# Optimization experiments

Hardware: AMD Instinct MI355X
Metric: run time of the kernel (lower is better)

## Reference

```python
import jax, jax.numpy as jnp
import numpy as np

BN_EPS = 1e-5

def setup_inputs() -> dict:
    key = jax.random.key(0)
    ks = jax.random.split(key, 8)
    C = 64
    NB, N_SP = 256, 64          # num blocks, spatial n (size3d = (1, 64, 64))
    N = NB * N_SP * N_SP        # 1,048,576 total rows
    s = np.sqrt(2.0 / C).astype(np.float32)   # kaiming_normal fan_in scale
    s2 = np.sqrt(2.0 / (2 * C)).astype(np.float32)
    return {
        "x":   jax.random.normal(ks[0], (N, C), jnp.float32),
        "w11": jax.random.normal(ks[1], (C, C), jnp.float32) * s,
        "b11": jnp.zeros((C,), jnp.float32),
        "w12": jax.random.normal(ks[2], (C, C), jnp.float32) * s,
        "b12": jnp.zeros((C,), jnp.float32),
        "w21": jax.random.normal(ks[3], (C, C), jnp.float32) * s,
        "b21": jnp.zeros((C,), jnp.float32),
        "w22": jax.random.normal(ks[4], (C, C), jnp.float32) * s,
        "b22": jnp.zeros((C,), jnp.float32),
        "uW1": jax.random.normal(ks[5], (2 * C, C), jnp.float32) * s2,
        "ub1": jnp.zeros((C,), jnp.float32),
        "g1":  jnp.ones((C,), jnp.float32),
        "be1": jnp.zeros((C,), jnp.float32),
        "uW2": jax.random.normal(ks[6], (C, C), jnp.float32) * s,
        "ub2": jnp.zeros((C,), jnp.float32),
        "g2":  jnp.ones((C,), jnp.float32),
        "be2": jnp.zeros((C,), jnp.float32),
        "num_blocks": NB,
        "blk_n": N_SP,
    }

def _block_mlp(h, params):
    # 1x1 Conv2d stack == per-position channel matmul; W is (out_ch, in_ch)
    for W, b in params:
        h = jax.nn.relu(jnp.einsum('bijc,oc->bijo', h, W) + b)
    return h

def _bn_relu(z, g, b):
    # BatchNorm1d, training mode: batch mean / biased batch var
    mu = jnp.mean(z, axis=0)
    var = jnp.var(z, axis=0)
    return jax.nn.relu((z - mu) * jax.lax.rsqrt(var + BN_EPS) * g + b)

def reference(x, w11, b11, w12, b12, w21, b21, w22, b22,
              uW1, ub1, g1, be1, uW2, ub2, g2, be2, num_blocks, blk_n):
    C = x.shape[-1]
    # uniform blocks: split + reshape to (b=1, n, n, C) -> fold into one array
    xb = x.reshape(num_blocks, blk_n, blk_n, C)          # NHWC (block, i, j, c)
    m1 = _block_mlp(xb, [(w11, b11), (w12, b12)])
    m2 = _block_mlp(xb, [(w21, b21), (w22, b22)])
    # torch.matmul over trailing spatial dims, batched over (block, channel)
    corr = jnp.einsum('bikc,bkjc->bijc', m1, m2)
    h = jnp.sqrt(jax.nn.relu(corr)).reshape(-1, C)
    h = jnp.concatenate([x, h], axis=1)                  # [N, 2C]
    h = _bn_relu(h @ uW1 + ub1, g1, be1)
    h = _bn_relu(h @ uW2 + ub2, g2, be2)
    return h + x
```

## Files before the change

kernel.cpp:

```cpp
#include <hip/hip_runtime.h>

#define NROWS   1048576
#define SBLK    4096

using bfrag = __attribute__((ext_vector_type(8))) short;
using ffrag = __attribute__((ext_vector_type(4))) float;
using uifrag = __attribute__((ext_vector_type(4))) unsigned;

__device__ __forceinline__ float bf2f(unsigned short u) {
    unsigned w = ((unsigned)u) << 16;
    return __builtin_bit_cast(float, w);
}
__device__ __forceinline__ unsigned short f2bf(float f) {
    unsigned u = __builtin_bit_cast(unsigned, f);
    u += 0x7fffu + ((u >> 16) & 1u);
    return (unsigned short)(u >> 16);
}
__device__ __forceinline__ short pk(float f) { return (short)f2bf(f); }
__device__ __forceinline__ unsigned cvtpk(float lo, float hi) {
    unsigned r;
    asm("v_cvt_pk_bf16_f32 %0, %1, %2" : "=v"(r) : "v"(lo), "v"(hi));
    return r;
}

__global__ void k_prep(const float* __restrict__ w11, const float* __restrict__ w12,
                       const float* __restrict__ w21, const float* __restrict__ w22,
                       const float* __restrict__ uW1, const float* __restrict__ uW2,
                       unsigned short* __restrict__ w11b, unsigned short* __restrict__ w12b,
                       unsigned short* __restrict__ w21b, unsigned short* __restrict__ w22b,
                       unsigned short* __restrict__ uW1bt, unsigned short* __restrict__ uW2bt)
{
    int t = threadIdx.x;
    for (int i = t; i < 4096; i += 256) {
        w11b[i] = f2bf(w11[i]);
        w12b[i] = f2bf(w12[i]);
        w21b[i] = f2bf(w21[i]);
        w22b[i] = f2bf(w22[i]);
        int o = i >> 6, c = i & 63;
        uW2bt[o * 64 + c] = f2bf(uW2[c * 64 + o]);
    }
    for (int i = t; i < 8192; i += 256) {
        int o = i >> 7, c = i & 127;
        uW1bt[o * 128 + c] = f2bf(uW1[c * 64 + o]);
    }
}

__global__ __launch_bounds__(256, 3) void k_mlp(
    const float* __restrict__ x,
    const unsigned short* __restrict__ w11b, const float* __restrict__ b11,
    const unsigned short* __restrict__ w12b, const float* __restrict__ b12,
    const unsigned short* __restrict__ w21b, const float* __restrict__ b21,
    const unsigned short* __restrict__ w22b, const float* __restrict__ b22,
    unsigned short* __restrict__ M1, unsigned short* __restrict__ M2)
{
    __shared__ unsigned short ts[4][64 * 72];
    const int t   = threadIdx.x;
    const int w   = t >> 6, ln = t & 63;
    const int col = ln & 15, q = ln >> 4;
    unsigned short* tsw = ts[w];

    const int nw = gridDim.x * 4;
    for (int tile = blockIdx.x * 4 + w; tile < NROWS / 64; tile += nw) {
        const int n0 = tile * 64;
        const int b = n0 >> 12, s0 = n0 & (SBLK - 1);

        bfrag ax[4][2];
        #pragma unroll
        for (int mt = 0; mt < 4; ++mt) {
            const float* xr = x + (size_t)(n0 + mt * 16 + col) * 64 + q * 8;
            #pragma unroll
            for (int kt = 0; kt < 2; ++kt) {
                float4 lo = *reinterpret_cast<const float4*>(xr + kt * 32);
                float4 hi = *reinterpret_cast<const float4*>(xr + kt * 32 + 4);
                uifrag u;
                u[0] = cvtpk(lo.x, lo.y);
                u[1] = cvtpk(lo.z, lo.w);
                u[2] = cvtpk(hi.x, hi.y);
                u[3] = cvtpk(hi.z, hi.w);
                ax[mt][kt] = __builtin_bit_cast(bfrag, u);
            }
        }

        #pragma unroll
        for (int br = 0; br < 2; ++br) {
            const unsigned short* wA = br ? w21b : w11b;
            const unsigned short* wB = br ? w22b : w12b;
            const float* bA = br ? b21 : b11;
            const float* bB = br ? b22 : b12;
            unsigned short* Mb = (br ? M2 : M1) + ((size_t)b << 18) + s0;

            bfrag  bw[4][2];
            float4 bsv[4];
            #pragma unroll
            for (int ot = 0; ot < 4; ++ot) {
                #pragma unroll
                for (int kt = 0; kt < 2; ++kt)
                    bw[ot][kt] = *reinterpret_cast<const bfrag*>(
                        wA + (ot * 16 + col) * 64 + kt * 32 + q * 8);
                bsv[ot] = *reinterpret_cast<const float4*>(bA + ot * 16 + q * 4);
            }
            #pragma unroll
            for (int mt = 0; mt < 4; ++mt) {
                #pragma unroll
                for (int ot = 0; ot < 4; ++ot) {
                    ffrag acc = {0.f, 0.f, 0.f, 0.f};
                    acc = __builtin_amdgcn_mfma_f32_16x16x32_bf16(bw[ot][0], ax[mt][0], acc, 0, 0, 0);
                    acc = __builtin_amdgcn_mfma_f32_16x16x32_bf16(bw[ot][1], ax[mt][1], acc, 0, 0, 0);
                    float4 bs = bsv[ot];
                    unsigned u0 = cvtpk(fmaxf(acc[0] + bs.x, 0.f), fmaxf(acc[1] + bs.y, 0.f));
                    unsigned u1 = cvtpk(fmaxf(acc[2] + bs.z, 0.f), fmaxf(acc[3] + bs.w, 0.f));
                    *reinterpret_cast<uint2*>(&tsw[(mt * 16 + col) * 72 + ot * 16 + q * 4]) =
                        make_uint2(u0, u1);
                }
            }
            #pragma unroll
            for (int ot = 0; ot < 4; ++ot) {
                #pragma unroll
                for (int kt = 0; kt < 2; ++kt)
                    bw[ot][kt] = *reinterpret_cast<const bfrag*>(
                        wB + (ot * 16 + col) * 64 + kt * 32 + q * 8);
                bsv[ot] = *reinterpret_cast<const float4*>(bB + ot * 16 + q * 4);
            }
            #pragma unroll
            for (int mt = 0; mt < 4; ++mt) {
                bfrag az0 = *reinterpret_cast<const bfrag*>(&tsw[(mt * 16 + col) * 72 + q * 8]);
                bfrag az1 = *reinterpret_cast<const bfrag*>(&tsw[(mt * 16 + col) * 72 + 32 + q * 8]);
                #pragma unroll
                for (int ot = 0; ot < 4; ++ot) {
                    ffrag acc = {0.f, 0.f, 0.f, 0.f};
                    acc = __builtin_amdgcn_mfma_f32_16x16x32_bf16(bw[ot][0], az0, acc, 0, 0, 0);
                    acc = __builtin_amdgcn_mfma_f32_16x16x32_bf16(bw[ot][1], az1, acc, 0, 0, 0);
                    float4 bs = bsv[ot];
                    unsigned u0 = cvtpk(fmaxf(acc[0] + bs.x, 0.f), fmaxf(acc[1] + bs.y, 0.f));
                    unsigned u1 = cvtpk(fmaxf(acc[2] + bs.z, 0.f), fmaxf(acc[3] + bs.w, 0.f));
                    unsigned short* mp = Mb + (size_t)(ot * 16 + q * 4) * SBLK + mt * 16 + col;
                    mp[0]        = (unsigned short)u0;
                    mp[SBLK]     = (unsigned short)(u0 >> 16);
                    mp[2 * SBLK] = (unsigned short)u1;
                    mp[3 * SBLK] = (unsigned short)(u1 >> 16);
                }
            }
        }
    }
}

__global__ __launch_bounds__(256, 4) void k_corr(
    unsigned short* __restrict__ M1, const unsigned short* __restrict__ M2)
{
    __shared__ unsigned short Bt[4][64 * 72];
    const int t   = threadIdx.x;
    const int w   = t >> 6, ln = t & 63;
    const int col = ln & 15, q = ln >> 4;
    const size_t cb = (size_t)blockIdx.x << 14;

    const int k = t >> 2, j0 = (t & 3) * 16;
    #pragma unroll
    for (int cc = 0; cc < 4; ++cc) {
        const unsigned short* Bc = M2 + cb + cc * 4096 + (size_t)k * 64 + j0;
        uint4 p0 = reinterpret_cast<const uint4*>(Bc)[0];
        uint4 p1 = reinterpret_cast<const uint4*>(Bc)[1];
        unsigned pv[8] = { p0.x, p0.y, p0.z, p0.w, p1.x, p1.y, p1.z, p1.w };
        #pragma unroll
        for (int m = 0; m < 8; ++m) {
            Bt[cc][(j0 + 2 * m) * 72 + k]     = (unsigned short)(pv[m] & 0xffff);
            Bt[cc][(j0 + 2 * m + 1) * 72 + k] = (unsigned short)(pv[m] >> 16);
        }
    }
    __syncthreads();

    #pragma unroll
    for (int cc = 0; cc < 4; ++cc) {
        unsigned short* Ac = M1 + cb + cc * 4096;
        bfrag a0 = *reinterpret_cast<const bfrag*>(Ac + (w * 16 + col) * 64 + q * 8);
        bfrag a1 = *reinterpret_cast<const bfrag*>(Ac + (w * 16 + col) * 64 + 32 + q * 8);
        #pragma unroll
        for (int nj = 0; nj < 4; ++nj) {
            bfrag bq0 = *reinterpret_cast<const bfrag*>(&Bt[cc][(nj * 16 + col) * 72 + q * 8]);
            bfrag bq1 = *reinterpret_cast<const bfrag*>(&Bt[cc][(nj * 16 + col) * 72 + 32 + q * 8]);
            ffrag acc = {0.f, 0.f, 0.f, 0.f};
            acc = __builtin_amdgcn_mfma_f32_16x16x32_bf16(a0, bq0, acc, 0, 0, 0);
            acc = __builtin_amdgcn_mfma_f32_16x16x32_bf16(a1, bq1, acc, 0, 0, 0);
            unsigned u0 = cvtpk(sqrtf(fmaxf(acc[0], 0.f)), sqrtf(fmaxf(acc[1], 0.f)));
            unsigned u1 = cvtpk(sqrtf(fmaxf(acc[2], 0.f)), sqrtf(fmaxf(acc[3], 0.f)));
            unsigned short* hp = Ac + (size_t)(w * 16 + q * 4) * 64 + nj * 16 + col;
            hp[0]   = (unsigned short)u0;
            hp[64]  = (unsigned short)(u0 >> 16);
            hp[128] = (unsigned short)u1;
            hp[192] = (unsigned short)(u1 >> 16);
        }
    }
}

__global__ __launch_bounds__(256) void k_fc1(
    const float* __restrict__ x, const unsigned short* __restrict__ H,
    const unsigned short* __restrict__ uW1bt, const float* __restrict__ ub1,
    unsigned short* __restrict__ Z1, float* __restrict__ sum1, float* __restrict__ sq1)
{
    __shared__ unsigned short hs[4][16 * 72];
    __shared__ float redS[4][64], redQ[4][64];
    const int t   = threadIdx.x;
    const int w   = t >> 6, ln = t & 63;
    const int col = ln & 15, q = ln >> 4;
    unsigned short* hsw = hs[w];

    bfrag bw[4][4];
    #pragma unroll
    for (int kt = 0; kt < 4; ++kt)
        #pragma unroll
        for (int ct = 0; ct < 4; ++ct)
            bw[kt][ct] = *reinterpret_cast<const bfrag*>(
                uW1bt + (ct * 16 + col) * 128 + kt * 32 + q * 8);
    float bias[4];
    #pragma unroll
    for (int ct = 0; ct < 4; ++ct) bias[ct] = ub1[ct * 16 + col];

    float sA[4] = {0, 0, 0, 0}, qA[4] = {0, 0, 0, 0};

    for (int blk = blockIdx.x; blk < NROWS / 64; blk += gridDim.x) {
        const int n0 = blk * 64;
        const int b = n0 >> 12, s0 = n0 & (SBLK - 1);

        {
            const unsigned short* hp = H + ((size_t)b << 18) + (size_t)ln * SBLK + s0 + w * 16;
            uint4 p0 = reinterpret_cast<const uint4*>(hp)[0];
            uint4 p1 = reinterpret_cast<const uint4*>(hp)[1];
            unsigned pv[8] = { p0.x, p0.y, p0.z, p0.w, p1.x, p1.y, p1.z, p1.w };
            #pragma unroll
            for (int m = 0; m < 8; ++m) {
                hsw[(2 * m + 0) * 72 + ln] = (unsigned short)(pv[m] & 0xffff);
                hsw[(2 * m + 1) * 72 + ln] = (unsigned short)(pv[m] >> 16);
            }
        }

        const int row = w * 16 + col;
        bfrag ax[2];
        #pragma unroll
        for (int kt = 0; kt < 2; ++kt) {
            const float* xp = x + (size_t)(n0 + row) * 64 + kt * 32 + q * 8;
            float4 lo = reinterpret_cast<const float4*>(xp)[0];
            float4 hi = reinterpret_cast<const float4*>(xp)[1];
            uifrag u;
            u[0] = cvtpk(lo.x, lo.y);
            u[1] = cvtpk(lo.z, lo.w);
            u[2] = cvtpk(hi.x, hi.y);
            u[3] = cvtpk(hi.z, hi.w);
            ax[kt] = __builtin_bit_cast(bfrag, u);
        }
        bfrag ah0 = *reinterpret_cast<const bfrag*>(&hsw[col * 72 + q * 8]);
        bfrag ah1 = *reinterpret_cast<const bfrag*>(&hsw[col * 72 + 32 + q * 8]);

        #pragma unroll
        for (int ct = 0; ct < 4; ++ct) {
            ffrag acc = {0.f, 0.f, 0.f, 0.f};
            acc = __builtin_amdgcn_mfma_f32_16x16x32_bf16(ax[0], bw[0][ct], acc, 0, 0, 0);
            acc = __builtin_amdgcn_mfma_f32_16x16x32_bf16(ax[1], bw[1][ct], acc, 0, 0, 0);
            acc = __builtin_amdgcn_mfma_f32_16x16x32_bf16(ah0,  bw[2][ct], acc, 0, 0, 0);
            acc = __builtin_amdgcn_mfma_f32_16x16x32_bf16(ah1,  bw[3][ct], acc, 0, 0, 0);
            #pragma unroll
            for (int r = 0; r < 4; ++r) {
                float v = acc[r] + bias[ct];
                Z1[(size_t)(n0 + w * 16 + q * 4 + r) * 64 + ct * 16 + col] = f2bf(v);
                sA[ct] += v; qA[ct] += v * v;
            }
        }
    }

    #pragma unroll
    for (int ct = 0; ct < 4; ++ct) {
        float s = sA[ct], qq = qA[ct];
        s  += __shfl_xor(s, 16);  s  += __shfl_xor(s, 32);
        qq += __shfl_xor(qq, 16); qq += __shfl_xor(qq, 32);
        if (q == 0) { redS[w][ct * 16 + col] = s; redQ[w][ct * 16 + col] = qq; }
    }
    __syncthreads();
    if (t < 64) {
        float S = redS[0][t] + redS[1][t] + redS[2][t] + redS[3][t];
        float Q = redQ[0][t] + redQ[1][t] + redQ[2][t] + redQ[3][t];
        atomicAdd(&sum1[t], S);
        atomicAdd(&sq1[t], Q);
    }
}

__global__ void k_final(const float* __restrict__ sum, const float* __restrict__ sq,
                        const float* __restrict__ g, const float* __restrict__ be,
                        float* __restrict__ scale, float* __restrict__ shift)
{
    int c = threadIdx.x;
    if (c < 64) {
        const float invN = 1.f / (float)NROWS;
        float mu  = sum[c] * invN;
        float var = sq[c] * invN - mu * mu;
        float rs  = rsqrtf(var + 1e-5f);
        float sc  = g[c] * rs;
        scale[c] = sc;
        shift[c] = be[c] - mu * sc;
    }
}

__global__ __launch_bounds__(256) void k_fc2(
    const unsigned short* __restrict__ Z1, const unsigned short* __restrict__ uW2bt,
    const float* __restrict__ ub2, const float* __restrict__ scale1,
    const float* __restrict__ shift1,
    unsigned short* __restrict__ Z2, float* __restrict__ sum2, float* __restrict__ sq2)
{
    __shared__ float redS[4][64], redQ[4][64];
    const int t   = threadIdx.x;
    const int w   = t >> 6, ln = t & 63;
    const int col = ln & 15, q = ln >> 4;

    bfrag bw[2][4];
    #pragma unroll
    for (int kt = 0; kt < 2; ++kt)
        #pragma unroll
        for (int ct = 0; ct < 4; ++ct)
            bw[kt][ct] = *reinterpret_cast<const bfrag*>(
                uW2bt + (ct * 16 + col) * 64 + kt * 32 + q * 8);
    float bias[4];
    #pragma unroll
    for (int ct = 0; ct < 4; ++ct) bias[ct] = ub2[ct * 16 + col];
    float sc[2][8], sh[2][8];
    #pragma unroll
    for (int kt = 0; kt < 2; ++kt)
        #pragma unroll
        for (int j = 0; j < 8; ++j) {
            int c = kt * 32 + q * 8 + j;
            sc[kt][j] = scale1[c];
            sh[kt][j] = shift1[c];
        }

    float sA[4] = {0, 0, 0, 0}, qA[4] = {0, 0, 0, 0};

    const int wg = blockIdx.x * 4 + w;
    const int stride = gridDim.x * 4;
    for (int tile = wg; tile < NROWS / 16; tile += stride) {
        const size_t rbase = (size_t)tile * 16;
        bfrag a[2];
        #pragma unroll
        for (int kt = 0; kt < 2; ++kt) {
            const unsigned short* zp = Z1 + (rbase + col) * 64 + kt * 32 + q * 8;
            uint4 p = *reinterpret_cast<const uint4*>(zp);
            unsigned pv[4] = { p.x, p.y, p.z, p.w };
            bfrag av;
            #pragma unroll
            for (int m = 0; m < 4; ++m) {
                float lo = bf2f((unsigned short)(pv[m] & 0xffff));
                float hi = bf2f((unsigned short)(pv[m] >> 16));
                lo = fmaxf(fmaf(lo, sc[kt][2 * m],     sh[kt][2 * m]),     0.f);
                hi = fmaxf(fmaf(hi, sc[kt][2 * m + 1], sh[kt][2 * m + 1]), 0.f);
                av[2 * m] = pk(lo); av[2 * m + 1] = pk(hi);
            }
            a[kt] = av;
        }
        #pragma unroll
        for (int ct = 0; ct < 4; ++ct) {
            ffrag acc = {0.f, 0.f, 0.f, 0.f};
            acc = __builtin_amdgcn_mfma_f32_16x16x32_bf16(a[0], bw[0][ct], acc, 0, 0, 0);
            acc = __builtin_amdgcn_mfma_f32_16x16x32_bf16(a[1], bw[1][ct], acc, 0, 0, 0);
            #pragma unroll
            for (int r = 0; r < 4; ++r) {
                float v = acc[r] + bias[ct];
                Z2[(rbase + q * 4 + r) * 64 + ct * 16 + col] = f2bf(v);
                sA[ct] += v; qA[ct] += v * v;
            }
        }
    }

    #pragma unroll
    for (int ct = 0; ct < 4; ++ct) {
        float s = sA[ct], qq = qA[ct];
        s  += __shfl_xor(s, 16);  s  += __shfl_xor(s, 32);
        qq += __shfl_xor(qq, 16); qq += __shfl_xor(qq, 32);
        if (q == 0) { redS[w][ct * 16 + col] = s; redQ[w][ct * 16 + col] = qq; }
    }
    __syncthreads();
    if (t < 64) {
        float S = redS[0][t] + redS[1][t] + redS[2][t] + redS[3][t];
        float Q = redQ[0][t] + redQ[1][t] + redQ[2][t] + redQ[3][t];
        atomicAdd(&sum2[t], S);
        atomicAdd(&sq2[t], Q);
    }
}

__global__ __launch_bounds__(256) void k_out(
    const float* __restrict__ x, const unsigned short* __restrict__ Z2,
    const float* __restrict__ scale2, const float* __restrict__ shift2,
    float* __restrict__ out)
{
    const int i  = blockIdx.x * 256 + threadIdx.x;
    const int c0 = (i & 15) * 4;
    float4 xv = reinterpret_cast<const float4*>(x)[i];
    ushort4 zv = reinterpret_cast<const ushort4*>(Z2)[i];
    float4 o;
    o.x = fmaxf(fmaf(bf2f(zv.x), scale2[c0 + 0], shift2[c0 + 0]), 0.f) + xv.x;
    o.y = fmaxf(fmaf(bf2f(zv.y), scale2[c0 + 1], shift2[c0 + 1]), 0.f) + xv.y;
    o.z = fmaxf(fmaf(bf2f(zv.z), scale2[c0 + 2], shift2[c0 + 2]), 0.f) + xv.z;
    o.w = fmaxf(fmaf(bf2f(zv.w), scale2[c0 + 3], shift2[c0 + 3]), 0.f) + xv.w;
    reinterpret_cast<float4*>(out)[i] = o;
}

extern "C" void kernel_launch(void* const* d_in, const int* in_sizes, int n_in,
                              void* d_out, int out_size, void* d_ws, size_t ws_size,
                              hipStream_t stream)
{
    const float* x   = (const float*)d_in[0];
    const float* w11 = (const float*)d_in[1];
    const float* b11 = (const float*)d_in[2];
    const float* w12 = (const float*)d_in[3];
    const float* b12 = (const float*)d_in[4];
    const float* w21 = (const float*)d_in[5];
    const float* b21 = (const float*)d_in[6];
    const float* w22 = (const float*)d_in[7];
    const float* b22 = (const float*)d_in[8];
    const float* uW1 = (const float*)d_in[9];
    const float* ub1 = (const float*)d_in[10];
    const float* g1  = (const float*)d_in[11];
    const float* be1 = (const float*)d_in[12];
    const float* uW2 = (const float*)d_in[13];
    const float* ub2 = (const float*)d_in[14];
    const float* g2  = (const float*)d_in[15];
    const float* be2 = (const float*)d_in[16];

    char* ws = (char*)d_ws;
    const size_t BUF = (size_t)NROWS * 64 * sizeof(unsigned short);
    unsigned short* B0 = (unsigned short*)ws;
    unsigned short* B1 = (unsigned short*)(ws + BUF);
    float* stats  = (float*)(ws + 2 * BUF);
    float* sum1   = stats;        float* sq1    = stats + 64;
    float* sum2   = stats + 128;  float* sq2    = stats + 192;
    float* scale1 = stats + 256;  float* shift1 = stats + 320;
    float* scale2 = stats + 384;  float* shift2 = stats + 448;
    unsigned short* wb = (unsigned short*)(ws + 2 * BUF + 2048);
    unsigned short* w11b  = wb;
    unsigned short* w12b  = wb + 4096;
    unsigned short* w21b  = wb + 8192;
    unsigned short* w22b  = wb + 12288;
    unsigned short* uW1bt = wb + 16384;
    unsigned short* uW2bt = wb + 24576;

    hipMemsetAsync(stats, 0, 256 * sizeof(float), stream);

    k_prep<<<1, 256, 0, stream>>>(w11, w12, w21, w22, uW1, uW2,
                                  w11b, w12b, w21b, w22b, uW1bt, uW2bt);
    k_mlp<<<2048, 256, 0, stream>>>(x, w11b, b11, w12b, b12, w21b, b21, w22b, b22, B0, B1);
    k_corr<<<4096, 256, 0, stream>>>(B0, B1);
    k_fc1<<<2048, 256, 0, stream>>>(x, B0, uW1bt, ub1, B1, sum1, sq1);
    k_final<<<1, 64, 0, stream>>>(sum1, sq1, g1, be1, scale1, shift1);
    k_fc2<<<2048, 256, 0, stream>>>(B1, uW2bt, ub2, scale1, shift1, B0, sum2, sq2);
    k_final<<<1, 64, 0, stream>>>(sum2, sq2, g2, be2, scale2, shift2);
    k_out<<<NROWS * 64 / 4 / 256, 256, 0, stream>>>(x, B0, scale2, shift2, (float*)d_out);
}
```

Baseline: 998.4 us.

## Stream MLP rows per subtile, fold bias into MFMA accumulator, per-wave corr

k_mlp now loads and converts x one 16-row subtile at a time instead of holding all four, keeps both layer weight fragments resident, and initializes the accumulator with the bias instead of adding it afterwards. This cuts per-wave LDS scratch from 64 to 16 rows and raises the occupancy hint from 3 to 4 blocks. k_corr now gives each wave one channel matrix, so it transposes its own B into its own LDS slice with packed 32-bit writes and no block barrier. The risk is that holding both weight sets raises register pressure, and the per-subtile loop may expose more global-load latency.

```diff
diff --git a/kernel.cpp b/kernel.cpp
--- a/kernel.cpp
+++ b/kernel.cpp
@@ -45,7 +45,7 @@
     }
 }
 
-__global__ __launch_bounds__(256, 3) void k_mlp(
+__global__ __launch_bounds__(256, 4) void k_mlp(
     const float* __restrict__ x,
     const unsigned short* __restrict__ w11b, const float* __restrict__ b11,
     const unsigned short* __restrict__ w12b, const float* __restrict__ b12,
@@ -53,7 +53,7 @@
     const unsigned short* __restrict__ w22b, const float* __restrict__ b22,
     unsigned short* __restrict__ M1, unsigned short* __restrict__ M2)
 {
-    __shared__ unsigned short ts[4][64 * 72];
+    __shared__ unsigned short ts[4][16 * 72];
     const int t   = threadIdx.x;
     const int w   = t >> 6, ln = t & 63;
     const int col = ln & 15, q = ln >> 4;
@@ -63,23 +63,6 @@
     for (int tile = blockIdx.x * 4 + w; tile < NROWS / 64; tile += nw) {
         const int n0 = tile * 64;
         const int b = n0 >> 12, s0 = n0 & (SBLK - 1);
-
-        bfrag ax[4][2];
-        #pragma unroll
-        for (int mt = 0; mt < 4; ++mt) {
-            const float* xr = x + (size_t)(n0 + mt * 16 + col) * 64 + q * 8;
-            #pragma unroll
-            for (int kt = 0; kt < 2; ++kt) {
-                float4 lo = *reinterpret_cast<const float4*>(xr + kt * 32);
-                float4 hi = *reinterpret_cast<const float4*>(xr + kt * 32 + 4);
-                uifrag u;
-                u[0] = cvtpk(lo.x, lo.y);
-                u[1] = cvtpk(lo.z, lo.w);
-                u[2] = cvtpk(hi.x, hi.y);
-                u[3] = cvtpk(hi.z, hi.w);
-                ax[mt][kt] = __builtin_bit_cast(bfrag, u);
-            }
-        }
 
         #pragma unroll
         for (int br = 0; br < 2; ++br) {
@@ -89,50 +72,63 @@
             const float* bB = br ? b22 : b12;
             unsigned short* Mb = (br ? M2 : M1) + ((size_t)b << 18) + s0;
 
-            bfrag  bw[4][2];
-            float4 bsv[4];
+            bfrag w1f[4][2], w2f[4][2];
             #pragma unroll
-            for (int ot = 0; ot < 4; ++ot) {
+            for (int ot = 0; ot < 4; ++ot)
                 #pragma unroll
-                for (int kt = 0; kt < 2; ++kt)
-                    bw[ot][kt] = *reinterpret_cast<const bfrag*>(
+                for (int kt = 0; kt < 2; ++kt) {
+                    w1f[ot][kt] = *reinterpret_cast<const bfrag*>(
                         wA + (ot * 16 + col) * 64 + kt * 32 + q * 8);
-                bsv[ot] = *reinterpret_cast<const float4*>(bA + ot * 16 + q * 4);
-            }
-            #pragma unroll
+                    w2f[ot][kt] = *reinterpret_cast<const bfrag*>(
+                        wB + (ot * 16 + col) * 64 + kt * 32 + q * 8);
+                }
+
             for (int mt = 0; mt < 4; ++mt) {
+                const float* xr = x + (size_t)(n0 + mt * 16 + col) * 64 + q * 8;
+                bfrag ax0, ax1;
+                {
+                    float4 lo = *reinterpret_cast<const float4*>(xr);
+                    float4 hi = *reinterpret_cast<const float4*>(xr + 4);
+                    uifrag u;
+                    u[0] = cvtpk(lo.x, lo.y);
+                    u[1] = cvtpk(lo.z, lo.w);
+                    u[2] = cvtpk(hi.x, hi.y);
+                    u[3] = cvtpk(hi.z, hi.w);
+                    ax0 = __builtin_bit_cast(bfrag, u);
+                }
+                {
+                    float4 lo = *reinterpret_cast<const float4*>(xr + 32);
+                    float4 hi = *reinterpret_cast<const float4*>(xr + 36);
+                    uifrag u;
+                    u[0] = cvtpk(lo.x, lo.y);
+                    u[1] = cvtpk(lo.z, lo.w);
+                    u[2] = cvtpk(hi.x, hi.y);
+                    u[3] = cvtpk(hi.z, hi.w);
+                    ax1 = __builtin_bit_cast(bfrag, u);
+                }
+
                 #pragma unroll
                 for (int ot = 0; ot < 4; ++ot) {
-                    ffrag acc = {0.f, 0.f, 0.f, 0.f};
-                    acc = __builtin_amdgcn_mfma_f32_16x16x32_bf16(bw[ot][0], ax[mt][0], acc, 0, 0, 0);
-                    acc = __builtin_amdgcn_mfma_f32_16x16x32_bf16(bw[ot][1], ax[mt][1], acc, 0, 0, 0);
-                    float4 bs = bsv[ot];
-                    unsigned u0 = cvtpk(fmaxf(acc[0] + bs.x, 0.f), fmaxf(acc[1] + bs.y, 0.f));
-                    unsigned u1 = cvtpk(fmaxf(acc[2] + bs.z, 0.f), fmaxf(acc[3] + bs.w, 0.f));
-                    *reinterpret_cast<uint2*>(&tsw[(mt * 16 + col) * 72 + ot * 16 + q * 4]) =
+                    float4 bv = *reinterpret_cast<const float4*>(bA + ot * 16 + q * 4);
+                    ffrag acc = {bv.x, bv.y, bv.z, bv.w};
+                    acc = __builtin_amdgcn_mfma_f32_16x16x32_bf16(w1f[ot][0], ax0, acc, 0, 0, 0);
+                    acc = __builtin_amdgcn_mfma_f32_16x16x32_bf16(w1f[ot][1], ax1, acc, 0, 0, 0);
+                    unsigned u0 = cvtpk(fmaxf(acc[0], 0.f), fmaxf(acc[1], 0.f));
+                    unsigned u1 = cvtpk(fmaxf(acc[2], 0.f), fmaxf(acc[3], 0.f));
+                    *reinterpret_cast<uint2*>(&tsw[col * 72 + ot * 16 + q * 4]) =
                         make_uint2(u0, u1);
                 }
-            }
-            #pragma unroll
-            for (int ot = 0; ot < 4; ++ot) {
-                #pragma unroll
-                for (int kt = 0; kt < 2; ++kt)
-                    bw[ot][kt] = *reinterpret_cast<const bfrag*>(
-                        wB + (ot * 16 + col) * 64 + kt * 32 + q * 8);
-                bsv[ot] = *reinterpret_cast<const float4*>(bB + ot * 16 + q * 4);
-            }
-            #pragma unroll
-            for (int mt = 0; mt < 4; ++mt) {
-                bfrag az0 = *reinterpret_cast<const bfrag*>(&tsw[(mt * 16 + col) * 72 + q * 8]);
-                bfrag az1 = *reinterpret_cast<const bfrag*>(&tsw[(mt * 16 + col) * 72 + 32 + q * 8]);
+                bfrag az0 = *reinterpret_cast<const bfrag*>(&tsw[col * 72 + q * 8]);
+                bfrag az1 = *reinterpret_cast<const bfrag*>(&tsw[col * 72 + 32 + q * 8]);
+
                 #pragma unroll
                 for (int ot = 0; ot < 4; ++ot) {
-                    ffrag acc = {0.f, 0.f, 0.f, 0.f};
-                    acc = __builtin_amdgcn_mfma_f32_16x16x32_bf16(bw[ot][0], az0, acc, 0, 0, 0);
-                    acc = __builtin_amdgcn_mfma_f32_16x16x32_bf16(bw[ot][1], az1, acc, 0, 0, 0);
-                    float4 bs = bsv[ot];
-                    unsigned u0 = cvtpk(fmaxf(acc[0] + bs.x, 0.f), fmaxf(acc[1] + bs.y, 0.f));
-                    unsigned u1 = cvtpk(fmaxf(acc[2] + bs.z, 0.f), fmaxf(acc[3] + bs.w, 0.f));
+                    float4 bv = *reinterpret_cast<const float4*>(bB + ot * 16 + q * 4);
+                    ffrag acc = {bv.x, bv.y, bv.z, bv.w};
+                    acc = __builtin_amdgcn_mfma_f32_16x16x32_bf16(w2f[ot][0], az0, acc, 0, 0, 0);
+                    acc = __builtin_amdgcn_mfma_f32_16x16x32_bf16(w2f[ot][1], az1, acc, 0, 0, 0);
+                    unsigned u0 = cvtpk(fmaxf(acc[0], 0.f), fmaxf(acc[1], 0.f));
+                    unsigned u1 = cvtpk(fmaxf(acc[2], 0.f), fmaxf(acc[3], 0.f));
                     unsigned short* mp = Mb + (size_t)(ot * 16 + q * 4) * SBLK + mt * 16 + col;
                     mp[0]        = (unsigned short)u0;
                     mp[SBLK]     = (unsigned short)(u0 >> 16);
@@ -151,38 +147,48 @@
     const int t   = threadIdx.x;
     const int w   = t >> 6, ln = t & 63;
     const int col = ln & 15, q = ln >> 4;
-    const size_t cb = (size_t)blockIdx.x << 14;
-
-    const int k = t >> 2, j0 = (t & 3) * 16;
-    #pragma unroll
-    for (int cc = 0; cc < 4; ++cc) {
-        const unsigned short* Bc = M2 + cb + cc * 4096 + (size_t)k * 64 + j0;
-        uint4 p0 = reinterpret_cast<const uint4*>(Bc)[0];
-        uint4 p1 = reinterpret_cast<const uint4*>(Bc)[1];
-        unsigned pv[8] = { p0.x, p0.y, p0.z, p0.w, p1.x, p1.y, p1.z, p1.w };
-        #pragma unroll
-        for (int m = 0; m < 8; ++m) {
-            Bt[cc][(j0 + 2 * m) * 72 + k]     = (unsigned short)(pv[m] & 0xffff);
-            Bt[cc][(j0 + 2 * m + 1) * 72 + k] = (unsigned short)(pv[m] >> 16);
-        }
-    }
-    __syncthreads();
-
-    #pragma unroll
-    for (int cc = 0; cc < 4; ++cc) {
-        unsigned short* Ac = M1 + cb + cc * 4096;
-        bfrag a0 = *reinterpret_cast<const bfrag*>(Ac + (w * 16 + col) * 64 + q * 8);
-        bfrag a1 = *reinterpret_cast<const bfrag*>(Ac + (w * 16 + col) * 64 + 32 + q * 8);
+    unsigned short* Bw = Bt[w];
+    const size_t cb = ((size_t)(blockIdx.x * 4 + w)) << 12;
+
+    {
+        const int a = ln & 31, half = ln >> 5;
+        const unsigned short* Bc = M2 + cb + (size_t)(2 * a) * 64 + half * 32;
+        uint4 r0a = reinterpret_cast<const uint4*>(Bc)[0];
+        uint4 r0b = reinterpret_cast<const uint4*>(Bc)[1];
+        uint4 r0c = reinterpret_cast<const uint4*>(Bc)[2];
+        uint4 r0d = reinterpret_cast<const uint4*>(Bc)[3];
+        uint4 r1a = reinterpret_cast<const uint4*>(Bc + 64)[0];
+        uint4 r1b = reinterpret_cast<const uint4*>(Bc + 64)[1];
+        uint4 r1c = reinterpret_cast<const uint4*>(Bc + 64)[2];
+        uint4 r1d = reinterpret_cast<const uint4*>(Bc + 64)[3];
+        unsigned p0[16] = { r0a.x, r0a.y, r0a.z, r0a.w, r0b.x, r0b.y, r0b.z, r0b.w,
+                            r0c.x, r0c.y, r0c.z, r0c.w, r0d.x, r0d.y, r0d.z, r0d.w };
+        unsigned p1[16] = { r1a.x, r1a.y, r1a.z, r1a.w, r1b.x, r1b.y, r1b.z, r1b.w,
+                            r1c.x, r1c.y, r1c.z, r1c.w, r1d.x, r1d.y, r1d.z, r1d.w };
+        #pragma unroll
+        for (int m = 0; m < 16; ++m) {
+            int j0 = half * 32 + 2 * m;
+            unsigned lo0 = p0[m] & 0xffffu, hi0 = p0[m] >> 16;
+            unsigned lo1 = p1[m] & 0xffffu, hi1 = p1[m] >> 16;
+            *reinterpret_cast<unsigned*>(&Bw[(size_t)j0 * 72 + 2 * a])       = lo0 | (lo1 << 16);
+            *reinterpret_cast<unsigned*>(&Bw[(size_t)(j0 + 1) * 72 + 2 * a]) = hi0 | (hi1 << 16);
+        }
+    }
+
+    unsigned short* Ac = M1 + cb;
+    for (int mi = 0; mi < 4; ++mi) {
+        bfrag a0 = *reinterpret_cast<const bfrag*>(Ac + (size_t)(mi * 16 + col) * 64 + q * 8);
+        bfrag a1 = *reinterpret_cast<const bfrag*>(Ac + (size_t)(mi * 16 + col) * 64 + 32 + q * 8);
         #pragma unroll
         for (int nj = 0; nj < 4; ++nj) {
-            bfrag bq0 = *reinterpret_cast<const bfrag*>(&Bt[cc][(nj * 16 + col) * 72 + q * 8]);
-            bfrag bq1 = *reinterpret_cast<const bfrag*>(&Bt[cc][(nj * 16 + col) * 72 + 32 + q * 8]);
+            bfrag bq0 = *reinterpret_cast<const bfrag*>(&Bw[(size_t)(nj * 16 + col) * 72 + q * 8]);
+            bfrag bq1 = *reinterpret_cast<const bfrag*>(&Bw[(size_t)(nj * 16 + col) * 72 + 32 + q * 8]);
             ffrag acc = {0.f, 0.f, 0.f, 0.f};
             acc = __builtin_amdgcn_mfma_f32_16x16x32_bf16(a0, bq0, acc, 0, 0, 0);
             acc = __builtin_amdgcn_mfma_f32_16x16x32_bf16(a1, bq1, acc, 0, 0, 0);
             unsigned u0 = cvtpk(sqrtf(fmaxf(acc[0], 0.f)), sqrtf(fmaxf(acc[1], 0.f)));
             unsigned u1 = cvtpk(sqrtf(fmaxf(acc[2], 0.f)), sqrtf(fmaxf(acc[3], 0.f)));
-            unsigned short* hp = Ac + (size_t)(w * 16 + q * 4) * 64 + nj * 16 + col;
+            unsigned short* hp = Ac + (size_t)(mi * 16 + q * 4) * 64 + nj * 16 + col;
             hp[0]   = (unsigned short)u0;
             hp[64]  = (unsigned short)(u0 >> 16);
             hp[128] = (unsigned short)u1;
```

After: 1.199 ms. 1.2x slower.
